# Performance work log

Hardware: AMD Instinct MI355X
Metric: run time of the kernel (lower is better)

## Reference

```python
import jax, jax.numpy as jnp
import numpy as np

PATCH_DIM = 256
TRANS_DIM = 256
K_PATCH = 8


def _gelu(x):
    return jax.nn.gelu(x, approximate=False)  # torch nn.GELU default is exact


def setup_inputs() -> dict:
    key = jax.random.key(0)
    ks = jax.random.split(key, 20)
    s = 0.02
    d, t = PATCH_DIM, TRANS_DIM
    return {
        "x": jax.random.normal(ks[0], (4, 4096, 3 + d), dtype=jnp.float32),
        # weights stored (in, out): y = x @ W + b  (equiv to torch Linear)
        "W_in": jax.random.normal(ks[1], (d, t), jnp.float32) * s,
        "b_in": jax.random.normal(ks[2], (t,), jnp.float32) * s,
        "Wq": jax.random.normal(ks[3], (t, t), jnp.float32) * s,
        "Wk": jax.random.normal(ks[4], (t, t), jnp.float32) * s,
        "Wv": jax.random.normal(ks[5], (t, t), jnp.float32) * s,
        "Wg1": jax.random.normal(ks[6], (t, t), jnp.float32) * s,
        "bg1": jax.random.normal(ks[7], (t,), jnp.float32) * s,
        "Wg2": jax.random.normal(ks[8], (t, t), jnp.float32) * s,
        "bg2": jax.random.normal(ks[9], (t,), jnp.float32) * s,
        "W_out": jax.random.normal(ks[10], (t, d), jnp.float32) * s,
        "b_out": jax.random.normal(ks[11], (d,), jnp.float32) * s,
        "Wp1": jax.random.normal(ks[12], (10, 128), jnp.float32) * s,
        "bp1": jax.random.normal(ks[13], (128,), jnp.float32) * s,
        "Wp2": jax.random.normal(ks[14], (128, t), jnp.float32) * s,
        "bp2": jax.random.normal(ks[15], (t,), jnp.float32) * s,
    }


def reference(x, W_in, b_in, Wq, Wk, Wv, Wg1, bg1, Wg2, bg2, W_out, b_out, Wp1, bp1, Wp2, bp2):
    centroid = x[:, :, :3]              # [B,S,3]
    pre = x[:, :, 3:]                   # [B,S,D]
    B, S, _ = centroid.shape
    scale = TRANS_DIM ** (-0.5)

    # square_distance: ||a-b||^2 = |a|^2 + |b|^2 - 2 a.b
    sq = jnp.sum(centroid * centroid, axis=-1)                     # [B,S]
    dist = sq[:, :, None] + sq[:, None, :] - 2.0 * jnp.einsum(
        "bsd,btd->bst", centroid, centroid)                        # [B,S,S]
    idx = jnp.argsort(dist, axis=-1)[:, :, :K_PATCH]               # [B,S,k]

    # index_points gather: [B,S,k,3]
    knn = jax.vmap(lambda c, i: c[i])(centroid, idx)
    ref_vec = knn - centroid[:, :, None, :]
    pos_struct = jnp.concatenate([
        jnp.broadcast_to(centroid[:, :, None, :], (B, S, K_PATCH, 3)),
        knn,
        ref_vec,
        jnp.linalg.norm(ref_vec, axis=-1, keepdims=True),
    ], axis=-1)                                                    # [B,S,k,10]

    pos_h = _gelu(pos_struct @ Wp1 + bp1) @ Wp2 + bp2              # [B,S,k,T]
    pos_emb = jnp.max(pos_h, axis=2)                               # [B,S,T]

    h = pre @ W_in + b_in + pos_emb                                # [B,S,T]
    q, k, v = h @ Wq, h @ Wk, h @ Wv
    attn = (_gelu((q - k) @ Wg1 + bg1) @ Wg2 + bg2) * scale
    attn = jax.nn.softmax(attn, axis=-1)                           # over feature dim
    res = attn * v
    return res @ W_out + b_out + pre                               # [B,S,D]
```

## Files before the change

### kernel.cpp

```cpp
#include <hip/hip_runtime.h>
#include <hip/hip_bf16.h>
#include <math.h>

#define S_   4096
#define XROW 259

typedef const float* fpp;
typedef __attribute__((ext_vector_type(8))) short   s8b;
typedef __attribute__((ext_vector_type(4))) float   f32x4;

__device__ __forceinline__ float us2f(unsigned short u){ return __uint_as_float(((unsigned)u)<<16); }
__device__ __forceinline__ unsigned short f2bu(float f){
  __hip_bfloat16 h = __float2bfloat16(f);
  return *reinterpret_cast<unsigned short*>(&h);
}
__device__ __forceinline__ unsigned short f2bt(float f){
  return (unsigned short)(__float_as_uint(f) >> 16);
}
__device__ __forceinline__ float gelu_f(float v){
  float u2 = 2.0f * v * fmaf(0.0356774081f, v*v, 0.7978845608f);
  float e  = __expf(u2);
  return v * (1.0f - __builtin_amdgcn_rcpf(e + 1.0f));
}

__global__ __launch_bounds__(256) void k_prep(
    fpp W_in, fpp Wq, fpp Wk, fpp Wv, fpp Wg1, fpp Wg2, fpp W_out, fpp Wp2, fpp Wp1,
    fpp x, unsigned short* __restrict__ FO, float4* __restrict__ cbuf)
{
  int bb = blockIdx.x, wv = threadIdx.x>>6, lane = threadIdx.x&63;
  if (bb < 192) {
    int m  = bb >> 5;
    int fi = (bb & 31)*4 + wv;
    int c = fi >> 3, s = fi & 7;
    int col = c*16 + (lane&15);
    int k0  = s*32 + (lane>>4)*8;
    fpp Wm = (m==0)?W_in:(m==2)?Wv:(m==3)?Wg1:(m==4)?Wg2:(m==5)?W_out:Wq;
    s8b v;
#pragma unroll
    for (int j=0;j<8;j++){
      float f = Wm[(size_t)(k0+j)*256 + col];
      if (m==1) f -= Wk[(size_t)(k0+j)*256 + col];
      v[j] = (short)f2bu(f);
    }
    *(s8b*)(FO + (size_t)m*65536 + (size_t)fi*512 + lane*8) = v;
  } else if (bb < 208) {
    int fi = (bb-192)*4 + wv;
    int c = fi >> 2, s = fi & 3;
    int col = c*16 + (lane&15);
    int k0  = s*32 + (lane>>4)*8;
    s8b v;
#pragma unroll
    for (int j=0;j<8;j++) v[j] = (short)f2bu(Wp2[(size_t)(k0+j)*256 + col]);
    *(s8b*)(FO + 393216 + (size_t)fi*512 + lane*8) = v;
  } else if (bb < 210) {
    int fi = (bb-208)*4 + wv;
    int col = fi*16 + (lane&15);
    int k0  = (lane>>4)*8;
    s8b v;
#pragma unroll
    for (int j=0;j<8;j++){
      int k = k0 + j;
      v[j] = (k < 10) ? (short)f2bu(Wp1[(size_t)k*128 + col]) : (short)0;
    }
    *(s8b*)(FO + 425984 + (size_t)fi*512 + lane*8) = v;
  } else {
    int t = (bb-210)*256 + threadIdx.x;
    size_t xrow = (size_t)t * XROW;
    float cx = x[xrow], cy = x[xrow+1], cz = x[xrow+2];
    cbuf[t] = make_float4(cx, cy, cz, 0.5f*fmaf(cz,cz,fmaf(cy,cy,cx*cx)) + 64.0f);
  }
}

__global__ __launch_bounds__(512,4) void k_knn(const float4* __restrict__ cbuf,
                                               unsigned short* __restrict__ idxw)
{
  __shared__ float4 cent4[S_];
  const int rowbase = blockIdx.x * 32;
  const int b = rowbase >> 12;
  const float4* cb = cbuf + (size_t)b*S_;
  for (int t = threadIdx.x; t < S_; t += 512) cent4[t] = cb[t];
  __syncthreads();
  const int r = threadIdx.x >> 4;
  const int L = threadIdx.x & 15;
  const int s = (rowbase & (S_-1)) + r;
  float4 cs = cent4[s];
  const float nsx = -cs.x, nsy = -cs.y, nsz = -cs.z;
  unsigned bk0=0xFFFFFFFFu, bk1=0xFFFFFFFFu, bk2=0xFFFFFFFFu;
  int t = L;
#pragma unroll 4
  for (int i = 0; i < 256; ++i) {
    float4 c = cent4[t];
    float m = fmaf(nsx, c.x, fmaf(nsy, c.y, fmaf(nsz, c.z, c.w)));
    unsigned kk = (__float_as_uint(m) & 0xFFFFF000u) | (unsigned)t;
    unsigned lo;
    lo = min(kk,bk0); kk = max(kk,bk0); bk0 = lo;
    lo = min(kk,bk1); kk = max(kk,bk1); bk1 = lo;
    bk2 = min(kk,bk2);
    t += 16;
  }
  size_t obase = (size_t)(rowbase + r) * 8;
  int h = 0;
#pragma unroll
  for (int round = 0; round < 8; ++round) {
    unsigned mdv = (h==0)?bk0:(h==1)?bk1:(h==2)?bk2:0xFFFFFFFFu;
    unsigned gd = mdv;
#pragma unroll
    for (int off=1; off<16; off<<=1)
      gd = min(gd, (unsigned)__shfl_xor((int)gd, off));
    if (L == 0) idxw[obase + round] = (unsigned short)(gd & 0xFFFu);
    h += (mdv == gd) ? 1 : 0;
  }
}

__global__ __launch_bounds__(512,4) void k_mega(
    fpp x, const unsigned short* __restrict__ idxw,
    fpp bp1, fpp bp2,
    const unsigned short* __restrict__ FO,
    fpp b_in, fpp bg1, fpp bg2, fpp b_out,
    float* __restrict__ out)
{
  __shared__ __align__(16) char pool[55296];
  __shared__ __align__(16) unsigned short pe[8448];
  unsigned short* X0 = (unsigned short*)pool;
  unsigned short* X1 = X0 + 8448;
  unsigned short* X2 = X1 + 8448;
  unsigned short (*psb)[40]  = (unsigned short (*)[40])pool;
  unsigned short (*hh)[136]  = (unsigned short (*)[136])(pool + 20480);

  const int tid = threadIdx.x, lane = tid & 63, wv = tid >> 6;
  const int arow = lane & 15, akb = lane >> 4, rbase = akb*4;
  const int ctb = wv*2;
  const int tok0 = blockIdx.x * 32, b = tok0 >> 12;
  const unsigned short* FO2 = FO + 393216;
  const unsigned short* FO3 = FO + 425984;
  const int col0 = ctb*16 + arow, col1 = col0 + 16;

  s8b bf3 = *(const s8b*)(FO3 + wv*512 + lane*8);
  float b1v = bp1[wv*16 + arow];
  float bp2v0 = bp2[col0], bp2v1 = bp2[col1];

  if (tid < 256) {
    int tk = tid >> 3;
    size_t grow = (size_t)(tok0 + tk), xrow = grow * XROW;
    float cx=x[xrow], cy=x[xrow+1], cz=x[xrow+2];
    int nb = idxw[grow*8 + (tid & 7)];
    size_t nrow = ((size_t)(b*S_ + nb)) * XROW;
    float nx=x[nrow], ny=x[nrow+1], nz=x[nrow+2];
    float rx=nx-cx, ry=ny-cy, rz=nz-cz;
    float nrm = sqrtf(fmaf(rz,rz,fmaf(ry,ry,rx*rx)));
    unsigned short* p = psb[tid];
    s8b v0 = { (short)f2bt(cx),(short)f2bt(cy),(short)f2bt(cz),(short)f2bt(nx),
               (short)f2bt(ny),(short)f2bt(nz),(short)f2bt(rx),(short)f2bt(ry) };
    s8b v1 = { (short)f2bt(rz),(short)f2bt(nrm),0,0,0,0,0,0 };
    s8b vz = { 0,0,0,0,0,0,0,0 };
    *(s8b*)(p) = v0; *(s8b*)(p+8) = v1; *(s8b*)(p+16) = vz; *(s8b*)(p+24) = vz;
  }
  __syncthreads();

  for (int c=0;c<2;++c){
#pragma unroll
    for (int rt=0;rt<8;++rt){
      s8b af = *(const s8b*)(&psb[c*128 + rt*16 + arow][akb*8]);
      f32x4 h4 = __builtin_amdgcn_mfma_f32_16x16x32_bf16(af, bf3, (f32x4){0.f,0.f,0.f,0.f}, 0,0,0);
#pragma unroll
      for (int rr=0;rr<4;++rr)
        hh[rt*16 + rbase + rr][wv*16 + arow] = f2bt(gelu_f(h4[rr] + b1v));
    }
    __syncthreads();
#pragma unroll
    for (int p=0;p<2;++p){
      f32x4 a2c[4][2];
#pragma unroll
      for (int rt=0;rt<4;++rt){ a2c[rt][0]=(f32x4){0.f,0.f,0.f,0.f}; a2c[rt][1]=(f32x4){0.f,0.f,0.f,0.f}; }
#pragma unroll
      for (int s=0;s<4;++s){
        s8b af0 = *(const s8b*)(&hh[p*64 +  0 + arow][s*32 + akb*8]);
        s8b af1 = *(const s8b*)(&hh[p*64 + 16 + arow][s*32 + akb*8]);
        s8b af2 = *(const s8b*)(&hh[p*64 + 32 + arow][s*32 + akb*8]);
        s8b af3v= *(const s8b*)(&hh[p*64 + 48 + arow][s*32 + akb*8]);
#pragma unroll
        for (int i=0;i<2;++i){
          s8b bf = *(const s8b*)(FO2 + ((size_t)((ctb+i)*4 + s))*512 + lane*8);
          a2c[0][i] = __builtin_amdgcn_mfma_f32_16x16x32_bf16(af0,  bf, a2c[0][i], 0,0,0);
          a2c[1][i] = __builtin_amdgcn_mfma_f32_16x16x32_bf16(af1,  bf, a2c[1][i], 0,0,0);
          a2c[2][i] = __builtin_amdgcn_mfma_f32_16x16x32_bf16(af2,  bf, a2c[2][i], 0,0,0);
          a2c[3][i] = __builtin_amdgcn_mfma_f32_16x16x32_bf16(af3v, bf, a2c[3][i], 0,0,0);
        }
      }
#pragma unroll
      for (int rt=0;rt<4;++rt)
#pragma unroll
        for (int i=0;i<2;++i){
          float pm = fmaxf(fmaxf(a2c[rt][i][0],a2c[rt][i][1]), fmaxf(a2c[rt][i][2],a2c[rt][i][3]));
          pm = fmaxf(pm, __shfl_xor(pm, 16));
          if ((akb & 1) == 0)
            pe[(c*16 + p*8 + rt*2 + (akb>>1))*264 + (ctb+i)*16 + arow] = f2bt(pm + (i ? bp2v1 : bp2v0));
        }
    }
    __syncthreads();
  }

#pragma unroll
  for (int p=0;p<2;++p){
    int i2 = p*512 + tid;
    int row = i2 >> 5, cb2 = i2 & 31;
    const float* src = x + (size_t)(tok0 + row)*XROW + 3 + cb2*8;
    s8b v;
#pragma unroll
    for (int j=0;j<8;j++) v[j] = (short)f2bt(src[j]);
    *(s8b*)(X0 + row*264 + cb2*8) = v;
  }
  __syncthreads();

  f32x4 acc[2][2];
  auto gphase = [&](const unsigned short* A, const unsigned short* FOm){
#pragma unroll
    for (int rt=0;rt<2;++rt){ acc[rt][0]=(f32x4){0.f,0.f,0.f,0.f}; acc[rt][1]=(f32x4){0.f,0.f,0.f,0.f}; }
#pragma unroll
    for (int s=0;s<8;++s){
      s8b a0 = *(const s8b*)(A + arow*264 + s*32 + akb*8);
      s8b a1 = *(const s8b*)(A + (16+arow)*264 + s*32 + akb*8);
#pragma unroll
      for (int i=0;i<2;++i){
        s8b bf = *(const s8b*)(FOm + ((size_t)((ctb+i)*8 + s))*512 + lane*8);
        acc[0][i] = __builtin_amdgcn_mfma_f32_16x16x32_bf16(a0, bf, acc[0][i], 0,0,0);
        acc[1][i] = __builtin_amdgcn_mfma_f32_16x16x32_bf16(a1, bf, acc[1][i], 0,0,0);
      }
    }
  };

  gphase(X0, FO);
#pragma unroll
  for (int i=0;i<2;++i){
    int col = i ? col1 : col0;
    float bi = b_in[col];
#pragma unroll
    for (int rt=0;rt<2;++rt)
#pragma unroll
      for (int rr=0;rr<4;++rr){
        int row = rt*16 + rbase + rr;
        X1[row*264 + col] = f2bt(acc[rt][i][rr] + bi + us2f(pe[row*264 + col]));
      }
  }
  __syncthreads();

  gphase(X1, FO + 65536);
#pragma unroll
  for (int i=0;i<2;++i){
    int col = i ? col1 : col0;
#pragma unroll
    for (int rt=0;rt<2;++rt)
#pragma unroll
      for (int rr=0;rr<4;++rr)
        X0[(rt*16 + rbase + rr)*264 + col] = f2bt(acc[rt][i][rr]);
  }
  __syncthreads();

  gphase(X0, FO + 196608);
#pragma unroll
  for (int i=0;i<2;++i){
    int col = i ? col1 : col0;
    float bi = bg1[col];
#pragma unroll
    for (int rt=0;rt<2;++rt)
#pragma unroll
      for (int rr=0;rr<4;++rr)
        X2[(rt*16 + rbase + rr)*264 + col] = f2bt(gelu_f(acc[rt][i][rr] + bi));
  }
  __syncthreads();

  gphase(X2, FO + 262144);
#pragma unroll
  for (int i=0;i<2;++i){
    int col = i ? col1 : col0;
    float bi = bg2[col];
#pragma unroll
    for (int rt=0;rt<2;++rt)
#pragma unroll
      for (int rr=0;rr<4;++rr)
        X0[(rt*16 + rbase + rr)*264 + col] = f2bt((acc[rt][i][rr] + bi) * 0.0625f);
  }
  __syncthreads();

  {
    int row = tid >> 4, li = tid & 15;
    unsigned short* rp = X0 + row*264 + li*16;
    uint4 u0 = *(uint4*)rp, u1 = *(uint4*)(rp + 8);
    float f[16];
    f[0]=us2f(u0.x&0xffff); f[1]=us2f(u0.x>>16); f[2]=us2f(u0.y&0xffff); f[3]=us2f(u0.y>>16);
    f[4]=us2f(u0.z&0xffff); f[5]=us2f(u0.z>>16); f[6]=us2f(u0.w&0xffff); f[7]=us2f(u0.w>>16);
    f[8]=us2f(u1.x&0xffff); f[9]=us2f(u1.x>>16); f[10]=us2f(u1.y&0xffff); f[11]=us2f(u1.y>>16);
    f[12]=us2f(u1.z&0xffff); f[13]=us2f(u1.z>>16); f[14]=us2f(u1.w&0xffff); f[15]=us2f(u1.w>>16);
    float mx = f[0];
#pragma unroll
    for (int i=1;i<16;i++) mx = fmaxf(mx, f[i]);
#pragma unroll
    for (int o=1;o<16;o<<=1) mx = fmaxf(mx, __shfl_xor(mx, o));
    float ssum = 0.f;
#pragma unroll
    for (int i=0;i<16;i++){ f[i] = __expf(f[i]-mx); ssum += f[i]; }
#pragma unroll
    for (int o=1;o<16;o<<=1) ssum += __shfl_xor(ssum, o);
    float inv = __builtin_amdgcn_rcpf(ssum);
    uint4 w0, w1;
    w0.x=f2bt(f[0]*inv) | ((unsigned)f2bt(f[1]*inv)<<16);
    w0.y=f2bt(f[2]*inv) | ((unsigned)f2bt(f[3]*inv)<<16);
    w0.z=f2bt(f[4]*inv) | ((unsigned)f2bt(f[5]*inv)<<16);
    w0.w=f2bt(f[6]*inv) | ((unsigned)f2bt(f[7]*inv)<<16);
    w1.x=f2bt(f[8]*inv) | ((unsigned)f2bt(f[9]*inv)<<16);
    w1.y=f2bt(f[10]*inv)| ((unsigned)f2bt(f[11]*inv)<<16);
    w1.z=f2bt(f[12]*inv)| ((unsigned)f2bt(f[13]*inv)<<16);
    w1.w=f2bt(f[14]*inv)| ((unsigned)f2bt(f[15]*inv)<<16);
    *(uint4*)rp = w0; *(uint4*)(rp+8) = w1;
  }
  __syncthreads();

  gphase(X1, FO + 131072);
#pragma unroll
  for (int i=0;i<2;++i){
    int col = i ? col1 : col0;
#pragma unroll
    for (int rt=0;rt<2;++rt)
#pragma unroll
      for (int rr=0;rr<4;++rr){
        int row = rt*16 + rbase + rr;
        X2[row*264 + col] = f2bt(us2f(X0[row*264 + col]) * acc[rt][i][rr]);
      }
  }
  __syncthreads();

  gphase(X2, FO + 327680);
#pragma unroll
  for (int i=0;i<2;++i){
    int col = i ? col1 : col0;
    float bo = b_out[col];
#pragma unroll
    for (int rt=0;rt<2;++rt)
#pragma unroll
      for (int rr=0;rr<4;++rr){
        size_t row = (size_t)(tok0 + rt*16 + rbase + rr);
        out[row*256 + col] = acc[rt][i][rr] + bo + x[row*XROW + 3 + col];
      }
  }
}

extern "C" void kernel_launch(void* const* d_in, const int* in_sizes, int n_in,
                              void* d_out, int out_size, void* d_ws, size_t ws_size,
                              hipStream_t stream)
{
  fpp x    = (fpp)d_in[0];
  fpp W_in = (fpp)d_in[1];  fpp b_in = (fpp)d_in[2];
  fpp Wq   = (fpp)d_in[3];  fpp Wk   = (fpp)d_in[4];  fpp Wv = (fpp)d_in[5];
  fpp Wg1  = (fpp)d_in[6];  fpp bg1  = (fpp)d_in[7];
  fpp Wg2  = (fpp)d_in[8];  fpp bg2  = (fpp)d_in[9];
  fpp W_out= (fpp)d_in[10]; fpp b_out= (fpp)d_in[11];
  fpp Wp1  = (fpp)d_in[12]; fpp bp1  = (fpp)d_in[13];
  fpp Wp2  = (fpp)d_in[14]; fpp bp2  = (fpp)d_in[15];

  char* ws = (char*)d_ws;
  unsigned short* idxw = (unsigned short*)ws;
  unsigned short* FO   = (unsigned short*)(ws + 262144);

  float4* cbuf = (float4*)((char*)d_out + 16515072);

  k_prep<<<274, 256, 0, stream>>>(W_in,Wq,Wk,Wv,Wg1,Wg2,W_out,Wp2,Wp1, x, FO, cbuf);
  k_knn <<<512, 512, 0, stream>>>(cbuf, idxw);
  k_mega<<<512, 512, 0, stream>>>(x, idxw, bp1, bp2, FO,
                                  b_in, bg1, bg2, b_out, (float*)d_out);
}
```

Measured before the change: 67.65 us.

## Fuse KNN search into the main kernel and drop the separate launch

The k-nearest-neighbour search moves from its own kernel into the start of k_mega. Each block loads the batch's centroid buffer into a shared pool aliased with later buffers and writes neighbour indices to shared memory instead of global. This removes a kernel launch and the global round trip for indices. In exchange shared memory per block grows to about 72KB, which may cut occupancy, and the KNN phase now runs serially before the MLP work in each block.

```diff
diff --git a/kernel.cpp b/kernel.cpp
--- a/kernel.cpp
+++ b/kernel.cpp
@@ -71,61 +71,22 @@
   }
 }
 
-__global__ __launch_bounds__(512,4) void k_knn(const float4* __restrict__ cbuf,
-                                               unsigned short* __restrict__ idxw)
-{
-  __shared__ float4 cent4[S_];
-  const int rowbase = blockIdx.x * 32;
-  const int b = rowbase >> 12;
-  const float4* cb = cbuf + (size_t)b*S_;
-  for (int t = threadIdx.x; t < S_; t += 512) cent4[t] = cb[t];
-  __syncthreads();
-  const int r = threadIdx.x >> 4;
-  const int L = threadIdx.x & 15;
-  const int s = (rowbase & (S_-1)) + r;
-  float4 cs = cent4[s];
-  const float nsx = -cs.x, nsy = -cs.y, nsz = -cs.z;
-  unsigned bk0=0xFFFFFFFFu, bk1=0xFFFFFFFFu, bk2=0xFFFFFFFFu;
-  int t = L;
-#pragma unroll 4
-  for (int i = 0; i < 256; ++i) {
-    float4 c = cent4[t];
-    float m = fmaf(nsx, c.x, fmaf(nsy, c.y, fmaf(nsz, c.z, c.w)));
-    unsigned kk = (__float_as_uint(m) & 0xFFFFF000u) | (unsigned)t;
-    unsigned lo;
-    lo = min(kk,bk0); kk = max(kk,bk0); bk0 = lo;
-    lo = min(kk,bk1); kk = max(kk,bk1); bk1 = lo;
-    bk2 = min(kk,bk2);
-    t += 16;
-  }
-  size_t obase = (size_t)(rowbase + r) * 8;
-  int h = 0;
-#pragma unroll
-  for (int round = 0; round < 8; ++round) {
-    unsigned mdv = (h==0)?bk0:(h==1)?bk1:(h==2)?bk2:0xFFFFFFFFu;
-    unsigned gd = mdv;
-#pragma unroll
-    for (int off=1; off<16; off<<=1)
-      gd = min(gd, (unsigned)__shfl_xor((int)gd, off));
-    if (L == 0) idxw[obase + round] = (unsigned short)(gd & 0xFFFu);
-    h += (mdv == gd) ? 1 : 0;
-  }
-}
-
 __global__ __launch_bounds__(512,4) void k_mega(
-    fpp x, const unsigned short* __restrict__ idxw,
+    fpp x, const float4* __restrict__ cbuf,
     fpp bp1, fpp bp2,
     const unsigned short* __restrict__ FO,
     fpp b_in, fpp bg1, fpp bg2, fpp b_out,
     float* __restrict__ out)
 {
-  __shared__ __align__(16) char pool[55296];
-  __shared__ __align__(16) unsigned short pe[8448];
+  __shared__ __align__(16) char pool[72192];
+  __shared__ __align__(8) unsigned short nbi[256];
+  float4* cent4 = (float4*)pool;
   unsigned short* X0 = (unsigned short*)pool;
   unsigned short* X1 = X0 + 8448;
   unsigned short* X2 = X1 + 8448;
   unsigned short (*psb)[40]  = (unsigned short (*)[40])pool;
   unsigned short (*hh)[136]  = (unsigned short (*)[136])(pool + 20480);
+  unsigned short* pe = (unsigned short*)(pool + 55296);
 
   const int tid = threadIdx.x, lane = tid & 63, wv = tid >> 6;
   const int arow = lane & 15, akb = lane >> 4, rbase = akb*4;
@@ -135,6 +96,45 @@
   const unsigned short* FO3 = FO + 425984;
   const int col0 = ctb*16 + arow, col1 = col0 + 16;
 
+  {
+    const float4* cb = cbuf + (size_t)b*S_;
+    for (int t = tid; t < S_; t += 512) cent4[t] = cb[t];
+  }
+  __syncthreads();
+
+  {
+    const int r = tid >> 4;
+    const int L = tid & 15;
+    const int s = (tok0 & (S_-1)) + r;
+    float4 cs = cent4[s];
+    const float nsx = -cs.x, nsy = -cs.y, nsz = -cs.z;
+    unsigned bk0=0xFFFFFFFFu, bk1=0xFFFFFFFFu, bk2=0xFFFFFFFFu;
+    int t = L;
+#pragma unroll 4
+    for (int i = 0; i < 256; ++i) {
+      float4 c = cent4[t];
+      float m = fmaf(nsx, c.x, fmaf(nsy, c.y, fmaf(nsz, c.z, c.w)));
+      unsigned kk = (__float_as_uint(m) & 0xFFFFF000u) | (unsigned)t;
+      unsigned lo;
+      lo = min(kk,bk0); kk = max(kk,bk0); bk0 = lo;
+      lo = min(kk,bk1); kk = max(kk,bk1); bk1 = lo;
+      bk2 = min(kk,bk2);
+      t += 16;
+    }
+    int h = 0;
+#pragma unroll
+    for (int round = 0; round < 8; ++round) {
+      unsigned mdv = (h==0)?bk0:(h==1)?bk1:(h==2)?bk2:0xFFFFFFFFu;
+      unsigned gd = mdv;
+#pragma unroll
+      for (int off=1; off<16; off<<=1)
+        gd = min(gd, (unsigned)__shfl_xor((int)gd, off));
+      if (L == 0) nbi[r*8 + round] = (unsigned short)(gd & 0xFFFu);
+      h += (mdv == gd) ? 1 : 0;
+    }
+  }
+  __syncthreads();
+
   s8b bf3 = *(const s8b*)(FO3 + wv*512 + lane*8);
   float b1v = bp1[wv*16 + arow];
   float bp2v0 = bp2[col0], bp2v1 = bp2[col1];
@@ -143,7 +143,7 @@
     int tk = tid >> 3;
     size_t grow = (size_t)(tok0 + tk), xrow = grow * XROW;
     float cx=x[xrow], cy=x[xrow+1], cz=x[xrow+2];
-    int nb = idxw[grow*8 + (tid & 7)];
+    int nb = nbi[tid];
     size_t nrow = ((size_t)(b*S_ + nb)) * XROW;
     float nx=x[nrow], ny=x[nrow+1], nz=x[nrow+2];
     float rx=nx-cx, ry=ny-cy, rz=nz-cz;
@@ -358,13 +358,10 @@
   fpp Wp2  = (fpp)d_in[14]; fpp bp2  = (fpp)d_in[15];
 
   char* ws = (char*)d_ws;
-  unsigned short* idxw = (unsigned short*)ws;
-  unsigned short* FO   = (unsigned short*)(ws + 262144);
-
-  float4* cbuf = (float4*)((char*)d_out + 16515072);
+  float4* cbuf        = (float4*)ws;
+  unsigned short* FO  = (unsigned short*)(ws + 262144);
 
   k_prep<<<274, 256, 0, stream>>>(W_in,Wq,Wk,Wv,Wg1,Wg2,W_out,Wp2,Wp1, x, FO, cbuf);
-  k_knn <<<512, 512, 0, stream>>>(cbuf, idxw);
-  k_mega<<<512, 512, 0, stream>>>(x, idxw, bp1, bp2, FO,
+  k_mega<<<512, 512, 0, stream>>>(x, cbuf, bp1, bp2, FO,
                                   b_in, bg1, bg2, b_out, (float*)d_out);
 }
```

New measurement: 64.33 us. 4.9% less time.
